# Performance work log

Hardware: AMD Instinct MI355X
Metric: run time of the kernel (lower is better)

The kernel has to match this reference:

```python
import jax, jax.numpy as jnp
import numpy as np

TEMP = 0.01            # entropy temperature
THRESH = 0.92          # hamming similarity threshold
BETA = 0.25            # commitment weight
ENT_W = 0.1            # entropy loss weight


def _l2_normalize(x, axis=-1, eps=1e-12):
    n = jnp.sqrt(jnp.sum(x * x, axis=axis, keepdims=True))
    return x / jnp.maximum(n, eps)


def _entropy_loss(affinity):
    # affinity: [N, K] codebook affinities (cosine similarities)
    fa = affinity / TEMP
    probs = jax.nn.softmax(fa, axis=-1)
    log_probs = jax.nn.log_softmax(fa + 1e-5, axis=-1)
    avg_probs = jnp.mean(probs, axis=0)
    avg_entropy = -jnp.sum(avg_probs * jnp.log(avg_probs + 1e-5))
    sample_entropy = -jnp.mean(jnp.sum(probs * log_probs, axis=-1))
    return sample_entropy - avg_entropy


def _hamming_consistency_loss(input_blocks, z_e):
    # binary occupancy: non-air voxels -> 1
    binary = (jnp.argmax(input_blocks, axis=1) != 0).astype(jnp.float32)  # [B,24,24,24]
    B = binary.shape[0]
    # faithful to torch: plain reshapes (no transpose)
    patterns = binary.reshape(B, 6, 4, 6, 4, 6, 4).reshape(B, 6, 6, 6, 64).reshape(-1, 64)
    N = patterns.shape[0]
    P = patterns
    # pairwise hamming distance via two Gram matmuls
    ham = P @ (1.0 - P).T + (1.0 - P) @ P.T          # [N,N]
    sim = 1.0 - ham / 64.0
    mask = (sim > THRESH) & (~jnp.eye(N, dtype=bool))
    W = jax.lax.stop_gradient(jnp.where(mask, sim, 0.0))  # detached weights
    # pre-quant embeddings per chunk, l2-normalized; cosine distance matrix
    emb = jnp.transpose(z_e, (0, 2, 3, 4, 1)).reshape(N, -1)  # [N, C]
    en = _l2_normalize(emb, axis=1)
    cos = en @ en.T                                   # [N,N]
    dist = 1.0 - cos
    return jnp.sum(dist * W) / (jnp.sum(W) + 1e-8)


def setup_inputs() -> dict:
    key = jax.random.key(0)
    k1, k2, k3 = jax.random.split(key, 3)
    input_blocks = jax.random.normal(k1, (16, 32, 24, 24, 24), dtype=jnp.float32)
    z_e = jax.random.normal(k2, (16, 256, 6, 6, 6), dtype=jnp.float32)
    codebook = jax.random.normal(k3, (1024, 256), dtype=jnp.float32)
    return {"input_blocks": input_blocks, "z_e": z_e, "codebook": codebook}


def reference(input_blocks, z_e, codebook):
    B, C, H, W, D = z_e.shape
    z = jnp.transpose(z_e, (0, 2, 3, 4, 1)).reshape(-1, C)   # [N, C]
    zn = _l2_normalize(z, axis=1)
    en = _l2_normalize(codebook, axis=1)                      # [K, C]
    affinity = zn @ en.T                                      # [N, K]
    idx = jnp.argmax(affinity, axis=1)                        # max cosine == min L2 on sphere
    z_q = en[idx]                                             # [N, C]
    sg = jax.lax.stop_gradient
    codebook_loss = jnp.mean((z_q - sg(zn)) ** 2)
    commit_loss = BETA * jnp.mean((sg(z_q) - zn) ** 2)
    ent_loss = ENT_W * _entropy_loss(affinity)
    ham_loss = _hamming_consistency_loss(input_blocks, z_e)
    loss = codebook_loss + commit_loss + ent_loss + ham_loss
    # straight-through estimator
    z_q_ste = zn + sg(z_q - zn)
    z_q_out = jnp.transpose(z_q_ste.reshape(B, H, W, D, C), (0, 4, 1, 2, 3))
    return z_q_out, loss, idx
```

## Files before the change

kernel.cpp:

```cpp
#include <hip/hip_runtime.h>
#include <cstdint>
#include <cstddef>

#define N_ROWS 3456
#define C_DIM 256
#define K_CB 1024
#define B_SZ 16
#define SPATIAL 216
#define VOX 13824
#define NCH 32
#define N_GBLK 108
#define N_FBLK 486

typedef __attribute__((ext_vector_type(16))) float f32x16;
typedef __attribute__((ext_vector_type(8))) short bf16x8;

__device__ __forceinline__ unsigned short f2bf_rne(float f) {
    unsigned int u = __float_as_uint(f);
    u += 0x7FFFu + ((u >> 16) & 1u);
    return (unsigned short)(u >> 16);
}
__device__ __forceinline__ float bf2f(unsigned short h) {
    unsigned int u = ((unsigned int)h) << 16;
    return __uint_as_float(u);
}

__device__ __forceinline__ size_t swz(int n, int c) {
    return (size_t)(n >> 5) * 8192 + (size_t)((c >> 3) * 256) + (size_t)((n & 31) * 8) + (c & 7);
}

__global__ __launch_bounds__(256) void k_pre(
        const float* __restrict__ in, const float* __restrict__ cb,
        const float* __restrict__ ze,
        unsigned long long* __restrict__ pats,
        float* __restrict__ scal,
        float* __restrict__ en,
        unsigned short* __restrict__ ehi, unsigned short* __restrict__ elo,
        unsigned short* __restrict__ zhi, unsigned short* __restrict__ zlo) {
    int bid = blockIdx.x;
    int t = threadIdx.x;
    if (bid < 864) {
        if (bid == 0 && t < 16) scal[t] = 0.0f;
        int v = bid * 256 + t;
        int b = v / VOX;
        int r = v % VOX;
        const float* p = in + (size_t)b * NCH * VOX + r;
        float v0 = p[0];
        float mx = -INFINITY;
#pragma unroll
        for (int c = 1; c < NCH; ++c) mx = fmaxf(mx, p[(size_t)c * VOX]);
        unsigned long long m = __ballot(mx > v0);
        if ((t & 63) == 0) pats[v >> 6] = m;
        return;
    }
    __shared__ float ws[16];
    if (bid < 1888) {
        int k = bid - 864, c = t;
        float v = cb[k * C_DIM + c];
        float ss = v * v;
#pragma unroll
        for (int off = 32; off > 0; off >>= 1) ss += __shfl_down(ss, off, 64);
        if ((c & 63) == 0) ws[c >> 6] = ss;
        __syncthreads();
        float nrm = fmaxf(sqrtf(ws[0] + ws[1] + ws[2] + ws[3]), 1e-12f);
        float o = v / nrm;
        en[k * C_DIM + c] = o;
        unsigned short h = f2bf_rne(o);
        size_t off = swz(k, c);
        ehi[off] = h;
        elo[off] = f2bf_rne(o - bf2f(h));
    } else {
        int zb = bid - 1888;
        int n0 = zb * 4;
        int b = n0 / SPATIAL, s0 = n0 - b * SPATIAL;
        int c = t, w = t >> 6, lane = t & 63;
        float4 v4 = *(const float4*)&ze[((size_t)(b * C_DIM + c)) * SPATIAL + s0];
        float q0 = v4.x * v4.x, q1 = v4.y * v4.y, q2 = v4.z * v4.z, q3 = v4.w * v4.w;
#pragma unroll
        for (int off = 32; off > 0; off >>= 1) {
            q0 += __shfl_down(q0, off, 64);
            q1 += __shfl_down(q1, off, 64);
            q2 += __shfl_down(q2, off, 64);
            q3 += __shfl_down(q3, off, 64);
        }
        if (lane == 0) {
            ws[w * 4 + 0] = q0; ws[w * 4 + 1] = q1;
            ws[w * 4 + 2] = q2; ws[w * 4 + 3] = q3;
        }
        __syncthreads();
        float vv[4] = {v4.x, v4.y, v4.z, v4.w};
#pragma unroll
        for (int j = 0; j < 4; ++j) {
            float nrm = fmaxf(sqrtf(ws[j] + ws[4 + j] + ws[8 + j] + ws[12 + j]), 1e-12f);
            float o = vv[j] / nrm;
            unsigned short h = f2bf_rne(o);
            size_t off = swz(n0 + j, c);
            zhi[off] = h;
            zlo[off] = f2bf_rne(o - bf2f(h));
        }
    }
}

__global__ __launch_bounds__(512) void k_fat(
        const unsigned short* __restrict__ zhi, const unsigned short* __restrict__ zlo,
        const unsigned short* __restrict__ ehi, const unsigned short* __restrict__ elo,
        const unsigned long long* __restrict__ pats,
        const float* __restrict__ en,
        float* __restrict__ avgp_part, float* __restrict__ scal,
        float* __restrict__ out) {
    __shared__ float zq[32 * 257];
    __shared__ float sm[32][8];
    __shared__ int   si[32][8];
    __shared__ float sS[32][8];
    __shared__ float sT[32][8];
    __shared__ float gm[32];
    __shared__ int   gmi[32];
    __shared__ float invS[32];
    __shared__ float ws8[8];
    __shared__ float hw8[8], hd8[8];
    __shared__ int lastflag;
    unsigned int* done = (unsigned int*)&scal[8];

    int t = threadIdx.x;
    int w = t >> 6, lane = t & 63;
    int half = lane >> 5, l31 = lane & 31;
    int bid = blockIdx.x;
    const bf16x8* __restrict__ Zh = (const bf16x8*)zhi;
    const bf16x8* __restrict__ Zl = (const bf16x8*)zlo;
    const bf16x8* __restrict__ Eh = (const bf16x8*)ehi;
    const bf16x8* __restrict__ El = (const bf16x8*)elo;

    if (bid < N_GBLK) {
        int sa = bid;
        int n0 = bid * 32;

        f32x16 acc[4];
#pragma unroll
        for (int q = 0; q < 4; ++q)
#pragma unroll
            for (int e = 0; e < 16; ++e) acc[q][e] = 0.0f;

#pragma unroll
        for (int s16 = 0; s16 < 16; ++s16) {
            int u = s16 * 64 + lane;
            bf16x8 ah = Zh[(size_t)sa * 1024 + u];
            bf16x8 al = Zl[(size_t)sa * 1024 + u];
            bf16x8 bh[4], bl[4];
#pragma unroll
            for (int q = 0; q < 4; ++q) {
                bh[q] = Eh[(size_t)(w * 4 + q) * 1024 + u];
                bl[q] = El[(size_t)(w * 4 + q) * 1024 + u];
            }
#pragma unroll
            for (int q = 0; q < 4; ++q) {
                acc[q] = __builtin_amdgcn_mfma_f32_32x32x16_bf16(ah, bh[q], acc[q], 0, 0, 0);
                acc[q] = __builtin_amdgcn_mfma_f32_32x32x16_bf16(ah, bl[q], acc[q], 0, 0, 0);
                acc[q] = __builtin_amdgcn_mfma_f32_32x32x16_bf16(al, bh[q], acc[q], 0, 0, 0);
            }
        }

#pragma unroll
        for (int g = 0; g < 16; ++g) {
            float m = acc[0][g];
            int mi = w * 128 + l31;
#pragma unroll
            for (int q = 1; q < 4; ++q) {
                float x = acc[q][g];
                int c = w * 128 + q * 32 + l31;
                if (x > m) { m = x; mi = c; }
            }
#pragma unroll
            for (int mask = 1; mask < 32; mask <<= 1) {
                float vo = __shfl_xor(m, mask, 64);
                int   io = __shfl_xor(mi, mask, 64);
                if (vo > m || (vo == m && io < mi)) { m = vo; mi = io; }
            }
            int row = (g & 3) + 8 * (g >> 2) + 4 * half;
            if (l31 == 0) { sm[row][w] = m; si[row][w] = mi; }
        }
        __syncthreads();

        float cmv = 0.0f;
        if (t < 32) {
            float m = sm[t][0];
            int mi = si[t][0];
#pragma unroll
            for (int ww = 1; ww < 8; ++ww) {
                float mw = sm[t][ww];
                int miw = si[t][ww];
                if (mw > m || (mw == m && miw < mi)) { m = mw; mi = miw; }
            }
            gm[t] = m; gmi[t] = mi;
            out[884737 + n0 + t] = (float)mi;
            cmv = 2.0f - 2.0f * m;
        }
        if (w == 0) {
#pragma unroll
            for (int off = 32; off > 0; off >>= 1) cmv += __shfl_down(cmv, off, 64);
            if (lane == 0) atomicAdd(&scal[1], cmv);
        }
        __syncthreads();

#pragma unroll
        for (int g = 0; g < 16; ++g) {
            int row = (g & 3) + 8 * (g >> 2) + 4 * half;
            float gmr = gm[row];
            float S = 0.0f, T = 0.0f;
#pragma unroll
            for (int q = 0; q < 4; ++q) {
                float d = 100.0f * (acc[q][g] - gmr);
                float ee = __expf(d);
                S += ee; T += ee * d;
                acc[q][g] = ee;
            }
#pragma unroll
            for (int mask = 1; mask < 32; mask <<= 1) {
                S += __shfl_xor(S, mask, 64);
                T += __shfl_xor(T, mask, 64);
            }
            if (l31 == 0) { sS[row][w] = S; sT[row][w] = T; }
        }
#pragma unroll
        for (int rr = 0; rr < 4; ++rr) {
            int row = w * 4 + rr;
            int mi = gmi[row];
            float4 g4 = *(const float4*)&en[(size_t)mi * C_DIM + lane * 4];
            zq[row * 257 + lane * 4 + 0] = g4.x;
            zq[row * 257 + lane * 4 + 1] = g4.y;
            zq[row * 257 + lane * 4 + 2] = g4.z;
            zq[row * 257 + lane * 4 + 3] = g4.w;
        }
        __syncthreads();

        float sev = 0.0f;
        if (t < 32) {
            float S = 0.0f, T = 0.0f;
#pragma unroll
            for (int ww = 0; ww < 8; ++ww) { S += sS[t][ww]; T += sT[t][ww]; }
            float iv = 1.0f / S;
            invS[t] = iv;
            sev = logf(S) - T * iv;
        }
        if (w == 0) {
#pragma unroll
            for (int off = 32; off > 0; off >>= 1) sev += __shfl_down(sev, off, 64);
            if (lane == 0) atomicAdd(&scal[0], sev);
        }
        __syncthreads();

        {
            float cs[4] = {0.0f, 0.0f, 0.0f, 0.0f};
#pragma unroll
            for (int g = 0; g < 16; ++g) {
                int row = (g & 3) + 8 * (g >> 2) + 4 * half;
                float iv = invS[row];
#pragma unroll
                for (int q = 0; q < 4; ++q) cs[q] += acc[q][g] * iv;
            }
#pragma unroll
            for (int q = 0; q < 4; ++q) cs[q] += __shfl_xor(cs[q], 32, 64);
            if (half == 0) {
#pragma unroll
                for (int q = 0; q < 4; ++q)
                    avgp_part[(size_t)bid * K_CB + w * 128 + q * 32 + l31] = cs[q];
            }
        }

        {
            int rl = t & 31, cg = t >> 5;
            int n = n0 + rl;
            int b = n / SPATIAL, s = n - b * SPATIAL;
            size_t obase = ((size_t)b * C_DIM) * SPATIAL + s;
#pragma unroll
            for (int cc = 0; cc < 16; ++cc) {
                int c = cg * 16 + cc;
                out[obase + (size_t)c * SPATIAL] = zq[rl * 257 + c];
            }
        }
    } else {
        int hb = bid - N_GBLK;
        int ti = 0, rem = hb;
        while (rem >= 27 - ti) { rem -= 27 - ti; ++ti; }
        int tj = ti + rem;
        int i0 = ti * 128, j0 = tj * 128;
        float factor = (ti == tj) ? 1.0f : 2.0f;
        int iw = w & 3, kh = w >> 2;
        int sib = ti * 4 + iw;
        int sjb = tj * 4;

        f32x16 acc[4];
#pragma unroll
        for (int c = 0; c < 4; ++c)
#pragma unroll
            for (int e = 0; e < 16; ++e) acc[c][e] = 0.0f;

#pragma unroll
        for (int s8 = 0; s8 < 8; ++s8) {
            int u = (kh * 8 + s8) * 64 + lane;
            bf16x8 a0 = Zh[(size_t)sib * 1024 + u];
            bf16x8 bf[4];
#pragma unroll
            for (int c = 0; c < 4; ++c)
                bf[c] = Zh[(size_t)(sjb + c) * 1024 + u];
#pragma unroll
            for (int c = 0; c < 4; ++c)
                acc[c] = __builtin_amdgcn_mfma_f32_32x32x16_bf16(a0, bf[c], acc[c], 0, 0, 0);
        }

        unsigned long long pj[4];
#pragma unroll
        for (int c = 0; c < 4; ++c) pj[c] = pats[j0 + c * 32 + l31];

        float sW = 0.0f, sD = 0.0f;
        int ibase = i0 + iw * 32 + 4 * half;
#pragma unroll
        for (int g = 0; g < 16; ++g) {
            int gi = ibase + (g & 3) + 8 * (g >> 2);
            unsigned long long pi = pats[gi];
#pragma unroll
            for (int c = 0; c < 4; ++c) {
                int gj = j0 + c * 32 + l31;
                int pop = __popcll(pi ^ pj[c]);
                float wgt = (pop <= 5 && gi != gj) ? (1.0f - (float)pop * 0.015625f) : 0.0f;
                sW += wgt;
                sD += wgt * acc[c][g];
            }
        }
#pragma unroll
        for (int off = 32; off > 0; off >>= 1) {
            sW += __shfl_down(sW, off, 64);
            sD += __shfl_down(sD, off, 64);
        }
        if (lane == 0) { hw8[w] = sW; hd8[w] = sD; }
        __syncthreads();
        if (t == 0) {
            float W = hw8[0] + hw8[1] + hw8[2] + hw8[3];
            float D = hd8[0] + hd8[1] + hd8[2] + hd8[3]
                    + hd8[4] + hd8[5] + hd8[6] + hd8[7];
            atomicAdd(&scal[2], factor * W);
            atomicAdd(&scal[3], factor * D);
        }
    }

    __syncthreads();
    if (t == 0) {
        __threadfence();
        unsigned int old = atomicAdd(done, 1u);
        lastflag = (old == N_FBLK - 1) ? 1 : 0;
    }
    __syncthreads();
    if (lastflag) {
        __threadfence();
        int col0 = t, col1 = t + 512;
        float p0 = 0.0f, p1 = 0.0f, p2 = 0.0f, p3 = 0.0f;
        float q0 = 0.0f, q1 = 0.0f, q2 = 0.0f, q3 = 0.0f;
        for (int bb = 0; bb < N_GBLK; bb += 4) {
            p0 += avgp_part[(size_t)(bb + 0) * K_CB + col0];
            p1 += avgp_part[(size_t)(bb + 1) * K_CB + col0];
            p2 += avgp_part[(size_t)(bb + 2) * K_CB + col0];
            p3 += avgp_part[(size_t)(bb + 3) * K_CB + col0];
            q0 += avgp_part[(size_t)(bb + 0) * K_CB + col1];
            q1 += avgp_part[(size_t)(bb + 1) * K_CB + col1];
            q2 += avgp_part[(size_t)(bb + 2) * K_CB + col1];
            q3 += avgp_part[(size_t)(bb + 3) * K_CB + col1];
        }
        float ap0 = (p0 + p1 + p2 + p3) * (1.0f / N_ROWS);
        float ap1 = (q0 + q1 + q2 + q3) * (1.0f / N_ROWS);
        float term = ap0 * logf(ap0 + 1e-5f) + ap1 * logf(ap1 + 1e-5f);
#pragma unroll
        for (int off = 32; off > 0; off >>= 1) term += __shfl_down(term, off, 64);
        if (lane == 0) ws8[w] = term;
        __syncthreads();
        if (t == 0) {
            float sAP = 0.0f;
#pragma unroll
            for (int i = 0; i < 8; ++i) sAP += ws8[i];
            float s0 = atomicAdd(&scal[0], 0.0f);
            float s1 = atomicAdd(&scal[1], 0.0f);
            float s2 = atomicAdd(&scal[2], 0.0f);
            float s3 = atomicAdd(&scal[3], 0.0f);
            float sample = s0 * (1.0f / N_ROWS);
            float commit = s1 * (1.0f / ((float)N_ROWS * C_DIM));
            float ent = 0.1f * (sample + sAP);
            float ham = (s2 - s3) / (s2 + 1e-8f);
            out[884736] = 1.25f * commit + ent + ham;
        }
    }
}

extern "C" void kernel_launch(void* const* d_in, const int* in_sizes, int n_in,
                              void* d_out, int out_size, void* d_ws, size_t ws_size,
                              hipStream_t stream) {
    const float* in_blocks = (const float*)d_in[0];
    const float* z_e       = (const float*)d_in[1];
    const float* cb        = (const float*)d_in[2];
    float* out = (float*)d_out;

    char* ws = (char*)d_ws;
    float* en   = (float*)(ws + 0);
    unsigned short* zhi = (unsigned short*)(ws + 15204352);
    unsigned short* zlo = (unsigned short*)(ws + 16973824);
    unsigned short* ehi = (unsigned short*)(ws + 18743296);
    unsigned short* elo = (unsigned short*)(ws + 19267584);
    unsigned long long* pats = (unsigned long long*)(ws + 19791872);
    float* avgp_part = (float*)(ws + 19819520);
    float* scal = (float*)(ws + 20704256);

    k_pre<<<2752, 256, 0, stream>>>(in_blocks, cb, z_e, pats, scal,
                                    en, ehi, elo, zhi, zlo);
    k_fat<<<N_FBLK, 512, 0, stream>>>(zhi, zlo, ehi, elo, pats, en,
                                      avgp_part, scal, out);
}
```

Baseline: 130.5 us.

## Split channel argmax across threads, widen pre blocks, drop fp32 codebook copy

The preprocessing kernel now uses 512-thread blocks. The occupancy-argmax path splits the 32 channels between two half-blocks, which raises memory-level parallelism per voxel. Codebook and z_e normalisation blocks each handle two rows or eight spatial positions, which cuts the grid size. The fp32 normalised codebook buffer is no longer written; the gather in the main kernel rebuilds z_q from the hi/lo bf16 split instead. This removes a 1 MB write and read, but the reconstructed z_q is only approximately equal to the fp32 value (hi+lo bf16) and adds an extra barrier in the argmax path.

```diff
diff --git a/kernel.cpp b/kernel.cpp
--- a/kernel.cpp
+++ b/kernel.cpp
@@ -29,52 +29,67 @@
     return (size_t)(n >> 5) * 8192 + (size_t)((c >> 3) * 256) + (size_t)((n & 31) * 8) + (c & 7);
 }
 
-__global__ __launch_bounds__(256) void k_pre(
+__global__ __launch_bounds__(512) void k_pre(
         const float* __restrict__ in, const float* __restrict__ cb,
         const float* __restrict__ ze,
         unsigned long long* __restrict__ pats,
         float* __restrict__ scal,
-        float* __restrict__ en,
         unsigned short* __restrict__ ehi, unsigned short* __restrict__ elo,
         unsigned short* __restrict__ zhi, unsigned short* __restrict__ zlo) {
     int bid = blockIdx.x;
     int t = threadIdx.x;
+    __shared__ float mx1[256];
+    __shared__ float ws[32];
     if (bid < 864) {
         if (bid == 0 && t < 16) scal[t] = 0.0f;
-        int v = bid * 256 + t;
+        int vl = t & 255, h = t >> 8;
+        int v = bid * 256 + vl;
         int b = v / VOX;
         int r = v % VOX;
-        const float* p = in + (size_t)b * NCH * VOX + r;
-        float v0 = p[0];
-        float mx = -INFINITY;
-#pragma unroll
-        for (int c = 1; c < NCH; ++c) mx = fmaxf(mx, p[(size_t)c * VOX]);
-        unsigned long long m = __ballot(mx > v0);
-        if ((t & 63) == 0) pats[v >> 6] = m;
+        const float* p = in + ((size_t)b * NCH + h * 16) * VOX + r;
+        float vals[16];
+#pragma unroll
+        for (int c = 0; c < 16; ++c) vals[c] = p[(size_t)c * VOX];
+        if (h == 1) {
+            float m = vals[0];
+#pragma unroll
+            for (int c = 1; c < 16; ++c) m = fmaxf(m, vals[c]);
+            mx1[vl] = m;
+        }
+        __syncthreads();
+        if (h == 0) {
+            float v0 = vals[0];
+            float m = vals[1];
+#pragma unroll
+            for (int c = 2; c < 16; ++c) m = fmaxf(m, vals[c]);
+            m = fmaxf(m, mx1[vl]);
+            unsigned long long bm = __ballot(m > v0);
+            if ((t & 63) == 0) pats[v >> 6] = bm;
+        }
         return;
     }
-    __shared__ float ws[16];
-    if (bid < 1888) {
-        int k = bid - 864, c = t;
+    int w = t >> 6, lane = t & 63;
+    if (bid < 1376) {
+        int h = t >> 8, c = t & 255;
+        int k = (bid - 864) * 2 + h;
         float v = cb[k * C_DIM + c];
         float ss = v * v;
 #pragma unroll
         for (int off = 32; off > 0; off >>= 1) ss += __shfl_down(ss, off, 64);
-        if ((c & 63) == 0) ws[c >> 6] = ss;
-        __syncthreads();
-        float nrm = fmaxf(sqrtf(ws[0] + ws[1] + ws[2] + ws[3]), 1e-12f);
+        if (lane == 0) ws[w] = ss;
+        __syncthreads();
+        float nrm = fmaxf(sqrtf(ws[h * 4 + 0] + ws[h * 4 + 1] + ws[h * 4 + 2] + ws[h * 4 + 3]), 1e-12f);
         float o = v / nrm;
-        en[k * C_DIM + c] = o;
-        unsigned short h = f2bf_rne(o);
+        unsigned short hh = f2bf_rne(o);
         size_t off = swz(k, c);
-        ehi[off] = h;
-        elo[off] = f2bf_rne(o - bf2f(h));
+        ehi[off] = hh;
+        elo[off] = f2bf_rne(o - bf2f(hh));
     } else {
-        int zb = bid - 1888;
-        int n0 = zb * 4;
+        int zb = bid - 1376;
+        int n0 = zb * 8;
         int b = n0 / SPATIAL, s0 = n0 - b * SPATIAL;
-        int c = t, w = t >> 6, lane = t & 63;
-        float4 v4 = *(const float4*)&ze[((size_t)(b * C_DIM + c)) * SPATIAL + s0];
+        int h = t >> 8, c = t & 255;
+        float4 v4 = *(const float4*)&ze[((size_t)(b * C_DIM + c)) * SPATIAL + s0 + h * 4];
         float q0 = v4.x * v4.x, q1 = v4.y * v4.y, q2 = v4.z * v4.z, q3 = v4.w * v4.w;
 #pragma unroll
         for (int off = 32; off > 0; off >>= 1) {
@@ -84,19 +99,23 @@
             q3 += __shfl_down(q3, off, 64);
         }
         if (lane == 0) {
-            ws[w * 4 + 0] = q0; ws[w * 4 + 1] = q1;
-            ws[w * 4 + 2] = q2; ws[w * 4 + 3] = q3;
+            int wi = w & 3;
+            ws[h * 16 + wi * 4 + 0] = q0;
+            ws[h * 16 + wi * 4 + 1] = q1;
+            ws[h * 16 + wi * 4 + 2] = q2;
+            ws[h * 16 + wi * 4 + 3] = q3;
         }
         __syncthreads();
         float vv[4] = {v4.x, v4.y, v4.z, v4.w};
 #pragma unroll
         for (int j = 0; j < 4; ++j) {
-            float nrm = fmaxf(sqrtf(ws[j] + ws[4 + j] + ws[8 + j] + ws[12 + j]), 1e-12f);
+            float nrm = fmaxf(sqrtf(ws[h * 16 + j] + ws[h * 16 + 4 + j] +
+                                    ws[h * 16 + 8 + j] + ws[h * 16 + 12 + j]), 1e-12f);
             float o = vv[j] / nrm;
-            unsigned short h = f2bf_rne(o);
-            size_t off = swz(n0 + j, c);
-            zhi[off] = h;
-            zlo[off] = f2bf_rne(o - bf2f(h));
+            unsigned short hh = f2bf_rne(o);
+            size_t off = swz(n0 + h * 4 + j, c);
+            zhi[off] = hh;
+            zlo[off] = f2bf_rne(o - bf2f(hh));
         }
     }
 }
@@ -105,7 +124,6 @@
         const unsigned short* __restrict__ zhi, const unsigned short* __restrict__ zlo,
         const unsigned short* __restrict__ ehi, const unsigned short* __restrict__ elo,
         const unsigned long long* __restrict__ pats,
-        const float* __restrict__ en,
         float* __restrict__ avgp_part, float* __restrict__ scal,
         float* __restrict__ out) {
     __shared__ float zq[32 * 257];
@@ -224,11 +242,13 @@
         for (int rr = 0; rr < 4; ++rr) {
             int row = w * 4 + rr;
             int mi = gmi[row];
-            float4 g4 = *(const float4*)&en[(size_t)mi * C_DIM + lane * 4];
-            zq[row * 257 + lane * 4 + 0] = g4.x;
-            zq[row * 257 + lane * 4 + 1] = g4.y;
-            zq[row * 257 + lane * 4 + 2] = g4.z;
-            zq[row * 257 + lane * 4 + 3] = g4.w;
+            size_t off = swz(mi, lane * 4);
+            const ushort4 h4 = *(const ushort4*)&ehi[off];
+            const ushort4 l4 = *(const ushort4*)&elo[off];
+            zq[row * 257 + lane * 4 + 0] = bf2f(h4.x) + bf2f(l4.x);
+            zq[row * 257 + lane * 4 + 1] = bf2f(h4.y) + bf2f(l4.y);
+            zq[row * 257 + lane * 4 + 2] = bf2f(h4.z) + bf2f(l4.z);
+            zq[row * 257 + lane * 4 + 3] = bf2f(h4.w) + bf2f(l4.w);
         }
         __syncthreads();
 
@@ -397,7 +417,6 @@
     float* out = (float*)d_out;
 
     char* ws = (char*)d_ws;
-    float* en   = (float*)(ws + 0);
     unsigned short* zhi = (unsigned short*)(ws + 15204352);
     unsigned short* zlo = (unsigned short*)(ws + 16973824);
     unsigned short* ehi = (unsigned short*)(ws + 18743296);
@@ -406,8 +425,8 @@
     float* avgp_part = (float*)(ws + 19819520);
     float* scal = (float*)(ws + 20704256);
 
-    k_pre<<<2752, 256, 0, stream>>>(in_blocks, cb, z_e, pats, scal,
-                                    en, ehi, elo, zhi, zlo);
-    k_fat<<<N_FBLK, 512, 0, stream>>>(zhi, zlo, ehi, elo, pats, en,
+    k_pre<<<1808, 512, 0, stream>>>(in_blocks, cb, z_e, pats, scal,
+                                    ehi, elo, zhi, zlo);
+    k_fat<<<N_FBLK, 512, 0, stream>>>(zhi, zlo, ehi, elo, pats,
                                       avgp_part, scal, out);
 }
```

Measured after the change: 129.2 us. Within noise of the previous version (-1.0%).
